# Performance work log

Hardware: AMD Instinct MI355X
Metric: run time of the kernel (lower is better)

## Reference

```python
import jax, jax.numpy as jnp
import numpy as np

NEG_SLOPE = 0.01  # torch LeakyReLU default


def gru_layer(x, w_ih, w_hh, b_ih, b_hh):
    # x: [T, B, in], weights per torch.nn.GRU convention: [3H, in]/[3H, H], gates (r,z,n)
    H = w_hh.shape[1]
    def step(h, x_t):
        gi = x_t @ w_ih.T + b_ih            # [B, 3H]
        gh = h @ w_hh.T + b_hh              # [B, 3H]
        i_r, i_z, i_n = jnp.split(gi, 3, axis=-1)
        h_r, h_z, h_n = jnp.split(gh, 3, axis=-1)
        r = jax.nn.sigmoid(i_r + h_r)
        z = jax.nn.sigmoid(i_z + h_z)
        n = jnp.tanh(i_n + r * h_n)
        h_new = (1.0 - z) * n + z * h
        return h_new, h_new
    h0 = jnp.zeros((x.shape[1], H), x.dtype)
    _, ys = jax.lax.scan(step, h0, x)
    return ys  # [T, B, H]


def setup_inputs() -> dict:
    key = jax.random.key(0)
    ks = jax.random.split(key, 16)
    T, B, V, H, L2 = 128, 2048, 64, 256, 100
    s = 1.0 / np.sqrt(H)
    d = {
        'tokens': jax.random.randint(ks[0], (T, B), 0, V, dtype=jnp.int32),
        'lens': jax.random.randint(ks[1], (B,), 0, T, dtype=jnp.int32),
        'emb': jax.random.normal(ks[2], (V, H), jnp.float32),
        'w_ih0': jax.random.normal(ks[3], (3 * H, H), jnp.float32) * s,
        'w_hh0': jax.random.normal(ks[4], (3 * H, H), jnp.float32) * s,
        'b_ih0': jax.random.normal(ks[5], (3 * H,), jnp.float32) * s,
        'b_hh0': jax.random.normal(ks[6], (3 * H,), jnp.float32) * s,
        'w_ih1': jax.random.normal(ks[7], (3 * H, H), jnp.float32) * s,
        'w_hh1': jax.random.normal(ks[8], (3 * H, H), jnp.float32) * s,
        'b_ih1': jax.random.normal(ks[9], (3 * H,), jnp.float32) * s,
        'b_hh1': jax.random.normal(ks[10], (3 * H,), jnp.float32) * s,
        'w1': jax.random.normal(ks[11], (H, H), jnp.float32) * s,
        'b1': jax.random.normal(ks[12], (H,), jnp.float32) * s,
        'w2': jax.random.normal(ks[13], (L2, H), jnp.float32) * s,
        'b2': jax.random.normal(ks[14], (L2,), jnp.float32) * s,
    }
    return d


def reference(tokens, lens, emb, w_ih0, w_hh0, b_ih0, b_hh0,
              w_ih1, w_hh1, b_ih1, b_hh1, w1, b1, w2, b2):
    x = emb[tokens]                                   # [T, B, H] embedding lookup
    h1 = gru_layer(x, w_ih0, w_hh0, b_ih0, b_hh0)     # layer 0
    h2 = gru_layer(h1, w_ih1, w_hh1, b_ih1, b_hh1)    # layer 1
    B = tokens.shape[1]
    out_t = h2[lens, jnp.arange(B)]                   # [B, H] gather per-example timestep
    z = out_t @ w1.T + b1
    z = jnp.where(z >= 0, z, NEG_SLOPE * z)           # LeakyReLU
    enc = z @ w2.T + b2                               # [B, 2*latent]
    return enc
```

## Files before the change

kernel.cpp:

```cpp
#include <hip/hip_runtime.h>
#include <hip/hip_bf16.h>

typedef __attribute__((ext_vector_type(8))) short bh8;
typedef __attribute__((ext_vector_type(4))) short sh4;
typedef __attribute__((ext_vector_type(4))) float f4;

static constexpr int T_STEPS = 128;
static constexpr int BTOT    = 2048;
static constexpr int HD      = 256;
static constexpr int NG      = 768;
static constexpr int LOUT    = 100;

__device__ __forceinline__ short f2bf(float f){
  unsigned u = __builtin_bit_cast(unsigned, f);
  unsigned r = (u + 0x7FFFu + ((u >> 16) & 1u)) >> 16;
  return (short)(unsigned short)r;
}
__device__ __forceinline__ float bf2f(short s){
  unsigned u = ((unsigned)(unsigned short)s) << 16;
  return __builtin_bit_cast(float, u);
}
__device__ __forceinline__ f4 mfma16(bh8 a, bh8 b, f4 c){
  return __builtin_amdgcn_mfma_f32_16x16x32_bf16(a, b, c, 0, 0, 0);
}
__device__ __forceinline__ float sigm(float x){
  return __builtin_amdgcn_rcpf(1.f + __expf(-x));
}
__device__ __forceinline__ float tanh_f(float x){
  return 1.f - 2.f*__builtin_amdgcn_rcpf(1.f + __expf(2.f*x));
}

__global__ void e0g_kernel(const float* __restrict__ emb, const float* __restrict__ w_ih0,
                           const float* __restrict__ b_ih0, const float* __restrict__ b_hh0,
                           short* __restrict__ E0g)
{
  int tid = blockIdx.x*blockDim.x + threadIdx.x;
  if (tid >= 64*NG) return;
  int v = tid / NG, n = tid % NG;
  const float4* er = (const float4*)(emb + (size_t)v*HD);
  const float4* wr = (const float4*)(w_ih0 + (size_t)n*HD);
  float s = 0.f;
#pragma unroll 4
  for (int k=0;k<HD/4;++k){
    float4 a = er[k], b = wr[k];
    s += a.x*b.x + a.y*b.y + a.z*b.z + a.w*b.w;
  }
  s += b_ih0[n];
  if (n < 512) s += b_hh0[n];
  int g = n >> 8, j = n & 255;
  int wid = j >> 5, c = (j >> 4) & 1, l15 = j & 15;
  E0g[(size_t)v*1024 + wid*128 + l15*8 + g*2 + c] = f2bf(s);
}

__global__ void pack_kernel(const float* __restrict__ w_hh0, const float* __restrict__ w_ih1,
                            const float* __restrict__ w_hh1, const float* __restrict__ w1,
                            const float* __restrict__ w2, short* __restrict__ pack)
{
  int tid = blockIdx.x*blockDim.x + threadIdx.x;
  if (tid >= 1336*64) return;
  int t = tid >> 6, lane = tid & 63;
  int l15 = lane & 15, lq = lane >> 4;
  const float* src = nullptr;
  bool zero = false;
  if (t < 1152){
    int m = t/384, tt = t%384, ct = tt/8, kt = tt%8;
    int n = ct*16 + l15;
    const float* Wm = (m==0) ? w_hh0 : (m==1 ? w_ih1 : w_hh1);
    src = Wm + (size_t)n*HD + kt*32 + lq*8;
  } else if (t < 1280){
    int tt = t - 1152, w = tt/16, rem = tt%16, ntt = rem/8, kt = rem%8;
    int n = w*32 + ntt*16 + l15;
    src = w1 + (size_t)n*HD + kt*32 + lq*8;
  } else {
    int tt = t - 1280, ntt = tt/8, kt = tt%8;
    int n = ntt*16 + l15;
    if (n < LOUT) src = w2 + (size_t)n*HD + kt*32 + lq*8;
    else zero = true;
  }
  bh8 o;
#pragma unroll
  for (int e=0;e<8;++e) o[e] = zero ? (short)0 : f2bf(src[e]);
  ((bh8*)pack)[tid] = o;
}


__device__ __forceinline__ void layer0_body(
    int bid, const int* __restrict__ tokens, const short* __restrict__ E0g,
    const short* __restrict__ pack, const float* __restrict__ b_hh0,
    short* __restrict__ s0c, short* __restrict__ h0g, int tc, int Tc,
    short (&st)[2][16*264])
{
  const int tid = threadIdx.x;
  const int wid = tid >> 6;
  const int lane = tid & 63;
  const int l15 = lane & 15, lq = lane >> 4;
  const int b0 = bid * 16;

  bh8 W[3][2][8];
  {
    const bh8* pt = (const bh8*)pack;
#pragma unroll
    for (int g=0;g<3;++g)
#pragma unroll
      for (int c=0;c<2;++c)
#pragma unroll
        for (int kt=0;kt<8;++kt)
          W[g][c][kt] = pt[(size_t)((g*16 + wid*2 + c)*8 + kt)*64 + lane];
  }
  float bhn0[2];
#pragma unroll
  for (int c=0;c<2;++c) bhn0[c] = b_hh0[512 + wid*32 + c*16 + l15];

  float h0s[2][4];
  if (tc == 0){
#pragma unroll
    for (int c=0;c<2;++c)
#pragma unroll
      for (int r=0;r<4;++r) h0s[c][r] = 0.f;
    for (int i=tid;i<16*264;i+=512) st[0][i] = 0;
  } else {
#pragma unroll
    for (int c=0;c<2;++c)
#pragma unroll
      for (int r=0;r<4;++r)
        h0s[c][r] = bf2f(h0g[(size_t)(b0 + lq*4 + r)*HD + wid*32 + c*16 + l15]);
    for (int i=tid;i<16*256;i+=512)
      st[0][(i>>8)*264 + (i&255)] = h0g[(size_t)(b0 + (i>>8))*HD + (i&255)];
  }

  const int e0base = wid*128 + l15*8;
  bh8 ev[4];
  {
    const int tg0 = tc*Tc;
    int tokr[4];
#pragma unroll
    for (int r=0;r<4;++r) tokr[r] = tokens[(size_t)tg0*BTOT + b0 + lq*4 + r];
#pragma unroll
    for (int r=0;r<4;++r)
      ev[r] = *(const bh8*)(E0g + (size_t)tokr[r]*1024 + e0base);
  }
  __syncthreads();

  const f4 zf = {0.f,0.f,0.f,0.f};
  const int crow = tid >> 5, ccol8 = (tid & 31)*8;

#pragma unroll 1
  for (int t=0; t<Tc; ++t){
    const int p = t & 1;
    const int tg = tc*Tc + t;
    const int tn = (tg+1 < T_STEPS) ? tg+1 : T_STEPS-1;
    int tokn[4];
#pragma unroll
    for (int r=0;r<4;++r) tokn[r] = tokens[(size_t)tn*BTOT + b0 + lq*4 + r];
    f4 acc[3][2];
#pragma unroll
    for (int g=0;g<3;++g){ acc[g][0]=zf; acc[g][1]=zf; }
    {
      const short* sp = &st[p][l15*264 + lq*8];
#pragma unroll
      for (int kt=0;kt<8;++kt){
        bh8 a = *(const bh8*)(sp + kt*32);
#pragma unroll
        for (int g=0;g<3;++g){
          acc[g][0] = mfma16(a, W[g][0][kt], acc[g][0]);
          acc[g][1] = mfma16(a, W[g][1][kt], acc[g][1]);
        }
      }
    }
    if (t > 0){
      bh8 cv = *(const bh8*)(&st[p][crow*264 + ccol8]);
      *(bh8*)(s0c + ((size_t)(t-1)*BTOT + b0 + crow)*HD + ccol8) = cv;
    }
    {
      short* stw = st[p^1];
#pragma unroll
      for (int c=0;c<2;++c){
        const int jh = wid*32 + c*16 + l15;
#pragma unroll
        for (int r4=0;r4<4;++r4){
          const int row = lq*4 + r4;
          const float er = bf2f(ev[r4][c]);
          const float ez = bf2f(ev[r4][2+c]);
          const float en = bf2f(ev[r4][4+c]);
          const float rg = sigm(acc[0][c][r4] + er);
          const float zg = sigm(acc[1][c][r4] + ez);
          const float ng = tanh_f(en + rg*(acc[2][c][r4] + bhn0[c]));
          const float h = ng + zg*(h0s[c][r4] - ng);
          h0s[c][r4] = h;
          stw[row*264 + jh] = f2bf(h);
        }
      }
    }
#pragma unroll
    for (int r=0;r<4;++r)
      ev[r] = *(const bh8*)(E0g + (size_t)tokn[r]*1024 + e0base);
    __syncthreads();
  }
  {
    bh8 cv = *(const bh8*)(&st[Tc & 1][crow*264 + ccol8]);
    *(bh8*)(s0c + ((size_t)(Tc-1)*BTOT + b0 + crow)*HD + ccol8) = cv;
    *(bh8*)(h0g + ((size_t)(b0 + crow))*HD + ccol8) = cv;
  }
}

__device__ __forceinline__ void layer1_body(
    int bid, const int* __restrict__ lens, const short* __restrict__ gi1p,
    const short* __restrict__ pack, const float* __restrict__ b_hh1,
    short* __restrict__ h1g, short* __restrict__ outbuf, int tc, int Tc,
    short (&st)[2][16*264])
{
  const int tid = threadIdx.x;
  const int wid = tid >> 6;
  const int lane = tid & 63;
  const int l15 = lane & 15, lq = lane >> 4;
  const int b0 = bid * 16;
  const int bblk = bid;

  bh8 W[3][2][8];
  {
    const bh8* pt = (const bh8*)pack;
#pragma unroll
    for (int g=0;g<3;++g)
#pragma unroll
      for (int c=0;c<2;++c)
#pragma unroll
        for (int kt=0;kt<8;++kt)
          W[g][c][kt] = pt[(size_t)(768 + (g*16 + wid*2 + c)*8 + kt)*64 + lane];
  }
  float bhn1[2];
#pragma unroll
  for (int c=0;c<2;++c) bhn1[c] = b_hh1[512 + wid*32 + c*16 + l15];

  int mylens[4];
#pragma unroll
  for (int r=0;r<4;++r) mylens[r] = lens[b0 + lq*4 + r];

  float h1s[2][4];
  if (tc == 0){
#pragma unroll
    for (int c=0;c<2;++c)
#pragma unroll
      for (int r=0;r<4;++r) h1s[c][r] = 0.f;
    for (int i=tid;i<16*264;i+=512) st[0][i] = 0;
  } else {
#pragma unroll
    for (int c=0;c<2;++c)
#pragma unroll
      for (int r=0;r<4;++r)
        h1s[c][r] = bf2f(h1g[(size_t)(b0 + lq*4 + r)*HD + wid*32 + c*16 + l15]);
    for (int i=tid;i<16*256;i+=512)
      st[0][(i>>8)*264 + (i&255)] = h1g[(size_t)(b0 + (i>>8))*HD + (i&255)];
  }

  bh8 gv[3];
#pragma unroll
  for (int g=0;g<3;++g)
    gv[g] = *(const bh8*)(gi1p + ((size_t)bblk*512 + tid)*24 + g*8);
  __syncthreads();

  const f4 zf = {0.f,0.f,0.f,0.f};
  const int crow = tid >> 5, ccol8 = (tid & 31)*8;

#pragma unroll 1
  for (int t=0; t<Tc; ++t){
    const int p = t & 1;
    const int tg = tc*Tc + t;
    f4 acc[3][2];
#pragma unroll
    for (int g=0;g<3;++g){ acc[g][0]=zf; acc[g][1]=zf; }
    {
      const short* sp = &st[p][l15*264 + lq*8];
#pragma unroll
      for (int kt=0;kt<8;++kt){
        bh8 a = *(const bh8*)(sp + kt*32);
#pragma unroll
        for (int g=0;g<3;++g){
          acc[g][0] = mfma16(a, W[g][0][kt], acc[g][0]);
          acc[g][1] = mfma16(a, W[g][1][kt], acc[g][1]);
        }
      }
    }
    {
      short* stw = st[p^1];
#pragma unroll
      for (int c=0;c<2;++c){
        const int jh = wid*32 + c*16 + l15;
#pragma unroll
        for (int r4=0;r4<4;++r4){
          const int row = lq*4 + r4;
          const float gr = bf2f(gv[0][c*4+r4]);
          const float gz = bf2f(gv[1][c*4+r4]);
          const float gn = bf2f(gv[2][c*4+r4]);
          const float rg = sigm(acc[0][c][r4] + gr);
          const float zg = sigm(acc[1][c][r4] + gz);
          const float ng = tanh_f(gn + rg*(acc[2][c][r4] + bhn1[c]));
          const float h = ng + zg*(h1s[c][r4] - ng);
          h1s[c][r4] = h;
          const short hb = f2bf(h);
          stw[row*264 + jh] = hb;
          if (tg == mylens[r4]) outbuf[(size_t)(b0 + row)*HD + jh] = hb;
        }
      }
    }
    if (t+1 < Tc){
#pragma unroll
      for (int g=0;g<3;++g)
        gv[g] = *(const bh8*)(gi1p + (((size_t)(t+1)*128 + bblk)*512 + tid)*24 + g*8);
    }
    __syncthreads();
  }
  {
    bh8 cv = *(const bh8*)(&st[Tc & 1][crow*264 + ccol8]);
    *(bh8*)(h1g + ((size_t)(b0 + crow))*HD + ccol8) = cv;
  }
}

__global__ __launch_bounds__(512, 1)
void scan_fat(const int* __restrict__ tokens, const short* __restrict__ E0g,
              const short* __restrict__ pack, const float* __restrict__ b_hh0,
              short* __restrict__ s0c, short* __restrict__ h0g,
              const int* __restrict__ lens, const short* __restrict__ gi1p,
              const float* __restrict__ b_hh1, short* __restrict__ h1g,
              short* __restrict__ outbuf, int tc0, int tc1, int Tc)
{
  __shared__ __align__(16) short st[2][16*264];
  const int bx = blockIdx.x;
  if (bx < 128){
    if (tc0 >= 0)
      layer0_body(bx, tokens, E0g, pack, b_hh0, s0c, h0g, tc0, Tc, st);
  } else {
    if (tc1 >= 0)
      layer1_body(bx - 128, lens, gi1p, pack, b_hh1, h1g, outbuf, tc1, Tc, st);
  }
}

__global__ __launch_bounds__(512, 1)
void gi1_gemm(const short* __restrict__ s0c, const short* __restrict__ pack,
              const float* __restrict__ b_ih1, const float* __restrict__ b_hh1,
              short* __restrict__ gi1p, int NC)
{
  const int tid = threadIdx.x;
  const int wid = tid >> 6;
  const int lane = tid & 63;
  const int l15 = lane & 15, lq = lane >> 4;

  __shared__ __align__(16) short ab[2][16*264];

  bh8 W[6][8];
#pragma unroll
  for (int i=0;i<6;++i)
#pragma unroll
    for (int kt=0;kt<8;++kt)
      W[i][kt] = ((const bh8*)pack)[(size_t)(384 + (wid*6+i)*8 + kt)*64 + lane];

  float bi[6];
  int offo[6];
#pragma unroll
  for (int i=0;i<6;++i){
    const int gc = (wid*6+i)*16 + l15;
    bi[i] = b_ih1[gc] + ((gc < 512) ? b_hh1[gc] : 0.f);
    const int g = gc >> 8, j = gc & 255;
    const int widp = j >> 5, c = (j >> 4) & 1;
    const int tidp = widp*64 + lq*16 + l15;
    offo[i] = tidp*24 + g*8 + c*4;
  }

  int ci = blockIdx.x;
  if (ci >= NC) return;
  bh8 sr = *(const bh8*)(s0c + (size_t)ci*4096 + tid*8);
  *(bh8*)(&ab[0][(tid>>5)*264 + (tid&31)*8]) = sr;
  __syncthreads();

  const f4 zf = {0.f,0.f,0.f,0.f};
  int p = 0;
#pragma unroll 1
  for (; ci < NC; ci += gridDim.x){
    const int cin = ci + (int)gridDim.x;
    const bool more = (cin < NC);
    if (more) sr = *(const bh8*)(s0c + (size_t)cin*4096 + tid*8);
    f4 acc[6];
#pragma unroll
    for (int i=0;i<6;++i) acc[i] = zf;
    const short* sp = &ab[p][l15*264 + lq*8];
#pragma unroll
    for (int kt=0;kt<8;++kt){
      bh8 a = *(const bh8*)(sp + kt*32);
#pragma unroll
      for (int i=0;i<6;++i) acc[i] = mfma16(a, W[i][kt], acc[i]);
    }
#pragma unroll
    for (int i=0;i<6;++i){
      sh4 v;
#pragma unroll
      for (int r4=0;r4<4;++r4) v[r4] = f2bf(acc[i][r4] + bi[i]);
      *(sh4*)(gi1p + (size_t)ci*512*24 + offo[i]) = v;
    }
    if (more)
      *(bh8*)(&ab[p^1][(tid>>5)*264 + (tid&31)*8]) = sr;
    p ^= 1;
    __syncthreads();
  }
}

__global__ __launch_bounds__(512, 1)
void head_kernel(const short* __restrict__ outbuf, const short* __restrict__ pack,
                 const float* __restrict__ b1, const float* __restrict__ b2,
                 float* __restrict__ out)
{
  const int tid = threadIdx.x;
  const int wid = tid >> 6;
  const int lane = tid & 63;
  const int l15 = lane & 15, lq = lane >> 4;
  const int b0 = blockIdx.x * 32;

  __shared__ __align__(16) short zA[32*264];
  __shared__ __align__(16) short zB[32*264];
  __shared__ float b1s[HD], b2s[112];
  if (tid < HD)  b1s[tid] = b1[tid];
  if (tid < 112) b2s[tid] = (tid < LOUT) ? b2[tid] : 0.f;

  for (int i=tid;i<32*256;i+=512){
    int row = i >> 8, col = i & 255;
    zA[row*264 + col] = outbuf[(size_t)(b0 + row)*HD + col];
  }
  __syncthreads();

  const f4 zf = {0.f,0.f,0.f,0.f};
  const int afrag = l15*264 + lq*8;
  constexpr int RT1 = 16*264;
  const bh8* packW1 = (const bh8*)pack + (size_t)(1152 + wid*16)*64 + lane;
  const bh8* packW2 = (const bh8*)pack + (size_t)(1280 + wid*8 )*64 + lane;

  {
    f4 az[2][2]; az[0][0]=zf; az[0][1]=zf; az[1][0]=zf; az[1][1]=zf;
#pragma unroll
    for (int kt=0;kt<8;++kt){
      bh8 a0 = *(const bh8*)(&zA[afrag + kt*32]);
      bh8 a1 = *(const bh8*)(&zA[afrag + RT1 + kt*32]);
#pragma unroll
      for (int nt=0;nt<2;++nt){
        bh8 b = packW1[(nt*8+kt)*64];
        az[nt][0] = mfma16(a0, b, az[nt][0]);
        az[nt][1] = mfma16(a1, b, az[nt][1]);
      }
    }
#pragma unroll
    for (int rt=0;rt<2;++rt)
#pragma unroll
      for (int nt=0;nt<2;++nt){
        const int jb = wid*32 + nt*16 + l15;
#pragma unroll
        for (int r4=0;r4<4;++r4){
          float v = az[nt][rt][r4] + b1s[jb];
          v = (v >= 0.f) ? v : 0.01f*v;
          zB[(rt*16+lq*4+r4)*264 + jb] = f2bf(v);
        }
      }
  }
  __syncthreads();

  if (wid < 7){
    f4 acc2[2]; acc2[0]=zf; acc2[1]=zf;
#pragma unroll
    for (int kt=0;kt<8;++kt){
      bh8 a0 = *(const bh8*)(&zB[afrag + kt*32]);
      bh8 a1 = *(const bh8*)(&zB[afrag + RT1 + kt*32]);
      bh8 b = packW2[kt*64];
      acc2[0] = mfma16(a0, b, acc2[0]);
      acc2[1] = mfma16(a1, b, acc2[1]);
    }
    const int n2 = wid*16 + l15;
    if (n2 < LOUT){
#pragma unroll
      for (int rt=0;rt<2;++rt)
#pragma unroll
        for (int r4=0;r4<4;++r4)
          out[(size_t)(b0 + rt*16 + lq*4 + r4)*LOUT + n2] = acc2[rt][r4] + b2s[n2];
    }
  }
}

extern "C" void kernel_launch(void* const* d_in, const int* in_sizes, int n_in,
                              void* d_out, int out_size, void* d_ws, size_t ws_size,
                              hipStream_t stream)
{
  const int*   tokens = (const int*)  d_in[0];
  const int*   lens   = (const int*)  d_in[1];
  const float* emb    = (const float*)d_in[2];
  const float* w_ih0  = (const float*)d_in[3];
  const float* w_hh0  = (const float*)d_in[4];
  const float* b_ih0  = (const float*)d_in[5];
  const float* b_hh0  = (const float*)d_in[6];
  const float* w_ih1  = (const float*)d_in[7];
  const float* w_hh1  = (const float*)d_in[8];
  const float* b_ih1  = (const float*)d_in[9];
  const float* b_hh1  = (const float*)d_in[10];
  const float* w1     = (const float*)d_in[11];
  const float* b1     = (const float*)d_in[12];
  const float* w2     = (const float*)d_in[13];
  const float* b2     = (const float*)d_in[14];

  char* ws = (char*)d_ws;
  size_t off = 0;
  short* pack = (short*)(ws + off); off += (size_t)1336*1024;
  short* E0g  = (short*)(ws + off); off += (size_t)64*1024*2;
  short* h0g  = (short*)(ws + off); off += (size_t)BTOT*HD*2;
  short* h1g  = (short*)(ws + off); off += (size_t)BTOT*HD*2;
  short* outb = (short*)(ws + off); off += (size_t)BTOT*HD*2;
  const size_t fixed = off;
  const size_t perT = (size_t)BTOT*HD*2 + (size_t)BTOT*NG*2;
  int Tc = T_STEPS;
  while (Tc > 1 && fixed + (size_t)Tc*perT > ws_size) Tc >>= 1;
  if (Tc > 32) Tc = 32;
  short* s0c  = (short*)(ws + fixed);
  short* gi1p = (short*)(ws + fixed + (size_t)Tc*BTOT*HD*2);

  e0g_kernel <<<(64*NG + 255)/256,   256, 0, stream>>>(emb, w_ih0, b_ih0, b_hh0, E0g);
  pack_kernel<<<(1336*64 + 255)/256, 256, 0, stream>>>(w_hh0, w_ih1, w_hh1, w1, w2, pack);

  const int nch = T_STEPS / Tc;
  for (int k = 0; k <= nch; ++k){
    const int tc0 = (k < nch) ? k : -1;
    const int tc1 = k - 1;
    scan_fat<<<256, 512, 0, stream>>>(tokens, E0g, pack, b_hh0, s0c, h0g,
                                      lens, gi1p, b_hh1, h1g, outb, tc0, tc1, Tc);
    if (k < nch)
      gi1_gemm<<<256, 512, 0, stream>>>(s0c, pack, b_ih1, b_hh1, gi1p, Tc*BTOT/16);
  }
  head_kernel<<<BTOT/32, 512, 0, stream>>>(outb, pack, b1, b2, (float*)d_out);
}
```

Measured before the change: 606.2 us.

## Fuse gi1 GEMM into scan kernel as third pipeline stage with double buffers

Folds the layer-1 input-projection GEMM into the fused scan kernel as a third group of 128 blocks, so layer-0 scan, the gi1 GEMM and the layer-1 scan for three consecutive chunks run concurrently. s0c and gi1p are double-buffered (A/B by chunk parity), and the separate gi1_gemm launch per chunk goes away. Tc is fixed at 16, which gives more chunks and launches but a shorter pipeline fill. The GEMM now uses only 128 blocks instead of 256, and the grid grows to 384 blocks, which on 256 CUs at one block per CU may not all be resident at the same time.

Result: slower. 647.9 us (+6.9%).

```diff
diff --git a/kernel.cpp b/kernel.cpp
--- a/kernel.cpp
+++ b/kernel.cpp
@@ -315,36 +315,15 @@
   }
 }
 
-__global__ __launch_bounds__(512, 1)
-void scan_fat(const int* __restrict__ tokens, const short* __restrict__ E0g,
-              const short* __restrict__ pack, const float* __restrict__ b_hh0,
-              short* __restrict__ s0c, short* __restrict__ h0g,
-              const int* __restrict__ lens, const short* __restrict__ gi1p,
-              const float* __restrict__ b_hh1, short* __restrict__ h1g,
-              short* __restrict__ outbuf, int tc0, int tc1, int Tc)
-{
-  __shared__ __align__(16) short st[2][16*264];
-  const int bx = blockIdx.x;
-  if (bx < 128){
-    if (tc0 >= 0)
-      layer0_body(bx, tokens, E0g, pack, b_hh0, s0c, h0g, tc0, Tc, st);
-  } else {
-    if (tc1 >= 0)
-      layer1_body(bx - 128, lens, gi1p, pack, b_hh1, h1g, outbuf, tc1, Tc, st);
-  }
-}
-
-__global__ __launch_bounds__(512, 1)
-void gi1_gemm(const short* __restrict__ s0c, const short* __restrict__ pack,
-              const float* __restrict__ b_ih1, const float* __restrict__ b_hh1,
-              short* __restrict__ gi1p, int NC)
+__device__ __forceinline__ void gi1_body(
+    int bid, const short* __restrict__ s0c, const short* __restrict__ pack,
+    const float* __restrict__ b_ih1, const float* __restrict__ b_hh1,
+    short* __restrict__ gi1p, int NC, short (&ab)[2][16*264])
 {
   const int tid = threadIdx.x;
   const int wid = tid >> 6;
   const int lane = tid & 63;
   const int l15 = lane & 15, lq = lane >> 4;
-
-  __shared__ __align__(16) short ab[2][16*264];
 
   bh8 W[6][8];
 #pragma unroll
@@ -365,7 +344,7 @@
     offo[i] = tidp*24 + g*8 + c*4;
   }
 
-  int ci = blockIdx.x;
+  int ci = bid;
   if (ci >= NC) return;
   bh8 sr = *(const bh8*)(s0c + (size_t)ci*4096 + tid*8);
   *(bh8*)(&ab[0][(tid>>5)*264 + (tid&31)*8]) = sr;
@@ -374,8 +353,8 @@
   const f4 zf = {0.f,0.f,0.f,0.f};
   int p = 0;
 #pragma unroll 1
-  for (; ci < NC; ci += gridDim.x){
-    const int cin = ci + (int)gridDim.x;
+  for (; ci < NC; ci += 128){
+    const int cin = ci + 128;
     const bool more = (cin < NC);
     if (more) sr = *(const bh8*)(s0c + (size_t)cin*4096 + tid*8);
     f4 acc[6];
@@ -399,6 +378,37 @@
       *(bh8*)(&ab[p^1][(tid>>5)*264 + (tid&31)*8]) = sr;
     p ^= 1;
     __syncthreads();
+  }
+}
+
+__global__ __launch_bounds__(512, 1)
+void scan_fat3(const int* __restrict__ tokens, const short* __restrict__ E0g,
+               const short* __restrict__ pack, const float* __restrict__ b_hh0,
+               short* __restrict__ s0cA, short* __restrict__ s0cB, short* __restrict__ h0g,
+               const int* __restrict__ lens,
+               short* __restrict__ gi1pA, short* __restrict__ gi1pB,
+               const float* __restrict__ b_ih1, const float* __restrict__ b_hh1,
+               short* __restrict__ h1g, short* __restrict__ outbuf,
+               int tc0, int tcg, int tc1, int Tc)
+{
+  __shared__ __align__(16) short st[2][16*264];
+  const int bx = blockIdx.x;
+  if (bx < 128){
+    if (tc0 >= 0){
+      short* s0c_w = (tc0 & 1) ? s0cB : s0cA;
+      layer0_body(bx, tokens, E0g, pack, b_hh0, s0c_w, h0g, tc0, Tc, st);
+    }
+  } else if (bx < 256){
+    if (tc1 >= 0){
+      const short* gi1p_r = (tc1 & 1) ? gi1pB : gi1pA;
+      layer1_body(bx - 128, lens, gi1p_r, pack, b_hh1, h1g, outbuf, tc1, Tc, st);
+    }
+  } else {
+    if (tcg >= 0){
+      const short* s0c_r = (tcg & 1) ? s0cB : s0cA;
+      short* gi1p_w = (tcg & 1) ? gi1pB : gi1pA;
+      gi1_body(bx - 256, s0c_r, pack, b_ih1, b_hh1, gi1p_w, Tc*128, st);
+    }
   }
 }
 
@@ -509,23 +519,27 @@
   short* outb = (short*)(ws + off); off += (size_t)BTOT*HD*2;
   const size_t fixed = off;
   const size_t perT = (size_t)BTOT*HD*2 + (size_t)BTOT*NG*2;
-  int Tc = T_STEPS;
-  while (Tc > 1 && fixed + (size_t)Tc*perT > ws_size) Tc >>= 1;
-  if (Tc > 32) Tc = 32;
-  short* s0c  = (short*)(ws + fixed);
-  short* gi1p = (short*)(ws + fixed + (size_t)Tc*BTOT*HD*2);
+  int Tc = 16;
+  while (Tc > 1 && fixed + (size_t)2*Tc*perT > ws_size) Tc >>= 1;
+  const size_t s0cE  = (size_t)Tc*BTOT*HD;
+  const size_t gi1pE = (size_t)Tc*BTOT*NG;
+  short* s0cA  = (short*)(ws + fixed);
+  short* s0cB  = s0cA  + s0cE;
+  short* gi1pA = s0cB  + s0cE;
+  short* gi1pB = gi1pA + gi1pE;
 
   e0g_kernel <<<(64*NG + 255)/256,   256, 0, stream>>>(emb, w_ih0, b_ih0, b_hh0, E0g);
   pack_kernel<<<(1336*64 + 255)/256, 256, 0, stream>>>(w_hh0, w_ih1, w_hh1, w1, w2, pack);
 
   const int nch = T_STEPS / Tc;
-  for (int k = 0; k <= nch; ++k){
+  for (int k = 0; k <= nch + 1; ++k){
     const int tc0 = (k < nch) ? k : -1;
-    const int tc1 = k - 1;
-    scan_fat<<<256, 512, 0, stream>>>(tokens, E0g, pack, b_hh0, s0c, h0g,
-                                      lens, gi1p, b_hh1, h1g, outb, tc0, tc1, Tc);
-    if (k < nch)
-      gi1_gemm<<<256, 512, 0, stream>>>(s0c, pack, b_ih1, b_hh1, gi1p, Tc*BTOT/16);
+    const int tcg = (k-1 >= 0 && k-1 < nch) ? k-1 : -1;
+    const int tc1 = (k-2 >= 0) ? k-2 : -1;
+    scan_fat3<<<384, 512, 0, stream>>>(tokens, E0g, pack, b_hh0,
+                                       s0cA, s0cB, h0g, lens,
+                                       gi1pA, gi1pB, b_ih1, b_hh1,
+                                       h1g, outb, tc0, tcg, tc1, Tc);
   }
   head_kernel<<<BTOT/32, 512, 0, stream>>>(outb, pack, b1, b2, (float*)d_out);
 }
```
